# Kernel optimization log

Hardware: AMD Instinct MI355X
Metric: run time of the kernel (lower is better)

Reference implementation:

```python
import jax, jax.numpy as jnp
import numpy as np

NODE_DIM = 256
EDGE_DIM = 128
NODE_IN = 768 + 769 + 4 + 1 + 3  # 1545


def setup_inputs() -> dict:
    key = jax.random.key(0)
    ks = jax.random.split(key, 16)
    B, N, H, W, C = 8, 128, 128, 128, 768
    obj_feats = jax.random.normal(ks[0], (B, N, 769), dtype=jnp.float32)
    masks = jax.random.uniform(ks[1], (B, N, H, W), dtype=jnp.float32)
    features = jax.random.normal(ks[2], (B, C, H, W), dtype=jnp.float32)
    bboxes = jax.random.uniform(ks[3], (B, N, 4), dtype=jnp.float32)
    conf = jax.random.uniform(ks[4], (B, N), dtype=jnp.float32)
    depth = jax.random.uniform(ks[5], (B, 1, H, W), dtype=jnp.float32) + 0.1
    # near-identity pose so homogeneous divide is well-conditioned
    pose = jnp.eye(4, dtype=jnp.float32)[None] + 0.01 * jax.random.normal(ks[6], (B, 4, 4), dtype=jnp.float32)
    s = 0.02
    node_w1 = s * jax.random.normal(ks[7], (512, NODE_IN), dtype=jnp.float32)
    node_b1 = jnp.zeros((512,), dtype=jnp.float32)
    node_w2 = s * jax.random.normal(ks[8], (NODE_DIM, 512), dtype=jnp.float32)
    node_b2 = jnp.zeros((NODE_DIM,), dtype=jnp.float32)
    edge_w1 = s * jax.random.normal(ks[9], (256, 2 * NODE_DIM), dtype=jnp.float32)
    edge_b1 = jnp.zeros((256,), dtype=jnp.float32)
    edge_w2 = s * jax.random.normal(ks[10], (EDGE_DIM, 256), dtype=jnp.float32)
    edge_b2 = jnp.zeros((EDGE_DIM,), dtype=jnp.float32)
    return dict(obj_feats=obj_feats, masks=masks, features=features, bboxes=bboxes,
                conf=conf, depth=depth, pose=pose,
                node_w1=node_w1, node_b1=node_b1, node_w2=node_w2, node_b2=node_b2,
                edge_w1=edge_w1, edge_b1=edge_b1, edge_w2=edge_w2, edge_b2=edge_b2)


def _forward(obj_feats, masks, features, bboxes, conf, depth, pose,
             node_w1, node_b1, node_w2, node_b2,
             edge_w1, edge_b1, edge_w2, edge_b2):
    B, C, H, W = features.shape
    N = masks.shape[1]
    K = jnp.eye(3, dtype=features.dtype)  # self.intrinsics

    # --- mask pooling: normalized mask-weighted average of features ---
    feats_flat = features.reshape(B, C, H * W)                 # [B,C,HW]
    m_flat = masks.reshape(B, N, H * W)                        # [B,N,HW]
    m_norm = m_flat / (m_flat.sum(-1, keepdims=True) + 1e-6)
    pooled = jnp.einsum('bnh,bch->bnc', m_norm, feats_flat)    # [B,N,C]

    # --- positional encoding ---
    x1, y1, x2, y2 = bboxes[..., 0], bboxes[..., 1], bboxes[..., 2], bboxes[..., 3]
    pos_feat = jnp.stack([(x1 + x2) / 2, (y1 + y2) / 2, x2 - x1, y2 - y1], axis=-1)  # [B,N,4]

    # --- motion prior ---
    ys = jnp.arange(H, dtype=masks.dtype)
    xs = jnp.arange(W, dtype=masks.dtype)
    mask_sum = masks.sum((-1, -2)) + 1e-6                      # [B,N]
    cx = jnp.einsum('bnhw,w->bn', masks, xs) / mask_sum
    cy = jnp.einsum('bnhw,h->bn', masks, ys) / mask_sum
    cx_idx = jnp.clip(jnp.round(cx).astype(jnp.int32), 0, W - 1)
    cy_idx = jnp.clip(jnp.round(cy).astype(jnp.int32), 0, H - 1)
    b_idx = jnp.arange(B)[:, None]                             # [B,1]
    z = depth[b_idx, 0, cy_idx, cx_idx]                        # [B,N]
    X = (cx - K[0, 2]) * z / K[0, 0]
    Y = (cy - K[1, 2]) * z / K[1, 1]
    ones = jnp.ones_like(z)
    P_h = jnp.stack([X, Y, z, ones], axis=-1)                  # [B,N,4]
    P_next = jnp.einsum('bij,bnj->bni', pose, P_h)             # [B,N,4]
    motion = P_next[..., :3] / P_next[..., 3:]                 # [B,N,3]

    # --- node MLP ---
    node_input = jnp.concatenate([pooled, obj_feats, pos_feat, conf[..., None], motion], axis=-1)
    h = jax.nn.relu(node_input @ node_w1.T + node_b1)
    node_emb = h @ node_w2.T + node_b2                         # [B,N,node_dim]

    # --- edge MLP: cat([n_i, n_j]) @ W1 == n_i @ W1a + n_j @ W1b (avoid O(N^2 * 2D) cat) ---
    D = node_emb.shape[-1]
    w1a, w1b = edge_w1[:, :D], edge_w1[:, D:]
    hi = node_emb @ w1a.T                                      # [B,N,256]
    hj = node_emb @ w1b.T                                      # [B,N,256]
    he = jax.nn.relu(hi[:, :, None, :] + hj[:, None, :, :] + edge_b1)  # [B,N,N,256]
    edge_emb = he @ edge_w2.T + edge_b2                        # [B,N,N,edge_dim]

    # --- adjacency: exp(-cdist) ---
    sq = jnp.sum(node_emb * node_emb, axis=-1)                 # [B,N]
    d2 = sq[:, :, None] + sq[:, None, :] - 2.0 * jnp.einsum('bnd,bmd->bnm', node_emb, node_emb)
    d2 = jnp.maximum(d2, 0.0)
    d = jnp.where(d2 > 0, jnp.sqrt(jnp.where(d2 > 0, d2, 1.0)), 0.0)  # grad-safe sqrt at 0
    adj = jnp.exp(-d)
    return node_emb, edge_emb, adj


def reference(obj_feats, masks, features, bboxes, conf, depth, pose,
              node_w1, node_b1, node_w2, node_b2,
              edge_w1, edge_b1, edge_w2, edge_b2):
    return _forward(obj_feats, masks, features, bboxes, conf, depth, pose,
                    node_w1, node_b1, node_w2, node_b2,
                    edge_w1, edge_b1, edge_w2, edge_b2)
```

## Files before the change

kernel.cpp:

```cpp
#include <hip/hip_runtime.h>
#include <hip/hip_bf16.h>

#define B_   8
#define N_   128
#define HW_  16384
#define C_   768
#define NIN_ 1545
#define NINP_ 1600
#define D1_  512
#define D_   256
#define EO_  128

typedef short s16x8 __attribute__((ext_vector_type(8)));
typedef float f32x16 __attribute__((ext_vector_type(16)));

__device__ __forceinline__ unsigned short f2bf(float x) {
  union { __hip_bfloat16 h; unsigned short u; } cv;
  cv.h = __float2bfloat16(x);
  return cv.u;
}

__global__ __launch_bounds__(256) void mask_stats_k(const float* __restrict__ masks,
                                                    const float* __restrict__ depth,
                                                    const float* __restrict__ pose,
                                                    float4* __restrict__ stats) {
  int row = blockIdx.x;
  int b = row >> 7;
  const float4* mp = (const float4*)(masks + (size_t)row * HW_);
  double s = 0.0, sx = 0.0, sy = 0.0;
  for (int it = 0; it < 16; ++it) {
    int i4 = threadIdx.x + it * 256;
    float4 v = mp[i4];
    int flat = i4 * 4;
    int y = flat >> 7, xb = flat & 127;
    double rs = (double)v.x + (double)v.y + (double)v.z + (double)v.w;
    s += rs;
    sx += (double)v.x * xb + (double)v.y * (xb + 1) + (double)v.z * (xb + 2) + (double)v.w * (xb + 3);
    sy += rs * (double)y;
  }
  for (int off = 32; off; off >>= 1) {
    s  += __shfl_down(s,  off);
    sx += __shfl_down(sx, off);
    sy += __shfl_down(sy, off);
  }
  __shared__ double red[3][4];
  int w = threadIdx.x >> 6, l = threadIdx.x & 63;
  if (l == 0) { red[0][w] = s; red[1][w] = sx; red[2][w] = sy; }
  __syncthreads();
  if (threadIdx.x == 0) {
    s  = red[0][0] + red[0][1] + red[0][2] + red[0][3];
    sx = red[1][0] + red[1][1] + red[1][2] + red[1][3];
    sy = red[2][0] + red[2][1] + red[2][2] + red[2][3];
    double msum = s + 1e-6;
    double cx = sx / msum, cy = sy / msum;
    int cxi = (int)rint(cx); cxi = min(127, max(0, cxi));
    int cyi = (int)rint(cy); cyi = min(127, max(0, cyi));
    double z = (double)depth[(size_t)b * HW_ + cyi * 128 + cxi];
    double Ph[4] = { cx * z, cy * z, z, 1.0 };
    const float* P = pose + b * 16;
    double pn[4];
    #pragma unroll
    for (int r = 0; r < 4; ++r)
      pn[r] = (double)P[r*4+0]*Ph[0] + (double)P[r*4+1]*Ph[1] + (double)P[r*4+2]*Ph[2] + (double)P[r*4+3]*Ph[3];
    double inv3 = 1.0 / pn[3];
    stats[row] = make_float4((float)(1.0 / msum), (float)(pn[0]*inv3), (float)(pn[1]*inv3), (float)(pn[2]*inv3));
  }
}

__global__ __launch_bounds__(256) void convw_k(const float* __restrict__ w1,
                                               const float* __restrict__ w2,
                                               const float* __restrict__ ew1,
                                               const float* __restrict__ ew2,
                                               unsigned short* __restrict__ w1b,
                                               unsigned short* __restrict__ w2b,
                                               unsigned short* __restrict__ we1b,
                                               unsigned short* __restrict__ ew2b) {
  int i = blockIdx.x * 256 + threadIdx.x;
  if (i < 512 * NINP_) {
    int r = i / NINP_, k = i - r * NINP_;
    w1b[i] = f2bf(k < NIN_ ? w1[r * NIN_ + k] : 0.0f);
    return;
  }
  i -= 512 * NINP_;
  if (i < 256 * 512) { w2b[i] = f2bf(w2[i]); return; }
  i -= 256 * 512;
  if (i < 512 * 256) {
    int r = i >> 8, k = i & 255;
    we1b[i] = f2bf(r < 256 ? ew1[r * 512 + k] : ew1[(r - 256) * 512 + 256 + k]);
    return;
  }
  i -= 512 * 256;
  if (i < 128 * 256) { ew2b[i] = f2bf(ew2[i]); }
}

__global__ __launch_bounds__(256) void pooled_k(const float* __restrict__ masks,
                                                const float* __restrict__ feats,
                                                float* __restrict__ Spart) {
  __shared__ short As[128 * 72];
  __shared__ short Bs[128 * 72];
  int bx = blockIdx.x;
  int ct = bx % 6, kc = bx / 6;
  int b = blockIdx.y;
  const float* mb = masks + (size_t)b * N_ * HW_;
  const float* fb = feats + ((size_t)b * C_ + (size_t)ct * 128) * HW_;
  int t = threadIdx.x, w = t >> 6, l = t & 63;
  int rsel = l & 31, khalf = l >> 5;
  f32x16 acc[4];
  #pragma unroll
  for (int nt = 0; nt < 4; ++nt)
    #pragma unroll
    for (int i = 0; i < 16; ++i) acc[nt][i] = 0.0f;

  for (int kt = 0; kt < 32; ++kt) {
    int kbase = kc * 2048 + kt * 64;
    #pragma unroll
    for (int c = 0; c < 8; ++c) {
      int chunk = t + 256 * c;
      int row = chunk >> 4;
      int kof = (chunk & 15) << 2;
      float4 va = *(const float4*)(mb + (size_t)row * HW_ + kbase + kof);
      ushort4 pa = { f2bf(va.x), f2bf(va.y), f2bf(va.z), f2bf(va.w) };
      *(ushort4*)((unsigned short*)As + row * 72 + kof) = pa;
      float4 vb = *(const float4*)(fb + (size_t)row * HW_ + kbase + kof);
      ushort4 pb = { f2bf(vb.x), f2bf(vb.y), f2bf(vb.z), f2bf(vb.w) };
      *(ushort4*)((unsigned short*)Bs + row * 72 + kof) = pb;
    }
    __syncthreads();
    #pragma unroll
    for (int ks = 0; ks < 4; ++ks) {
      s16x8 a = *(const s16x8*)&As[(w * 32 + rsel) * 72 + ks * 16 + khalf * 8];
      #pragma unroll
      for (int nt = 0; nt < 4; ++nt) {
        s16x8 bf = *(const s16x8*)&Bs[(nt * 32 + rsel) * 72 + ks * 16 + khalf * 8];
        acc[nt] = __builtin_amdgcn_mfma_f32_32x32x16_bf16(a, bf, acc[nt], 0, 0, 0);
      }
    }
    __syncthreads();
  }
  float* op = Spart + (size_t)kc * (B_ * N_ * C_ / 8 * 8) / 8 * 8;
  op = Spart + (size_t)kc * 786432 + (size_t)b * 98304;
  #pragma unroll
  for (int nt = 0; nt < 4; ++nt)
    #pragma unroll
    for (int reg = 0; reg < 16; ++reg) {
      int rm = w * 32 + (reg & 3) + 8 * (reg >> 2) + 4 * khalf;
      int cn = ct * 128 + nt * 32 + rsel;
      op[rm * C_ + cn] = acc[nt][reg];
    }
}

__global__ __launch_bounds__(256) void assemble_k(const float* __restrict__ Spart,
                                                  const float4* __restrict__ stats,
                                                  const float* __restrict__ obj,
                                                  const float* __restrict__ bboxes,
                                                  const float* __restrict__ conf,
                                                  unsigned short* __restrict__ ni) {
  int r = blockIdx.x;
  float4 st = stats[r];
  float x1 = bboxes[r*4+0], y1 = bboxes[r*4+1], x2 = bboxes[r*4+2], y2 = bboxes[r*4+3];
  for (int k = threadIdx.x; k < NINP_; k += 256) {
    float v;
    if (k < 768) {
      float acc = 0.0f;
      #pragma unroll
      for (int kc = 0; kc < 8; ++kc) acc += Spart[(size_t)kc * 786432 + (size_t)r * C_ + k];
      v = acc * st.x;
    } else if (k < 1537) v = obj[(size_t)r * 769 + (k - 768)];
    else if (k == 1537) v = 0.5f * (x1 + x2);
    else if (k == 1538) v = 0.5f * (y1 + y2);
    else if (k == 1539) v = x2 - x1;
    else if (k == 1540) v = y2 - y1;
    else if (k == 1541) v = conf[r];
    else if (k == 1542) v = st.y;
    else if (k == 1543) v = st.z;
    else if (k == 1544) v = st.w;
    else v = 0.0f;
    ni[(size_t)r * NINP_ + k] = f2bf(v);
  }
}

template <bool RELU, bool BIAS, int OUTM>
__global__ __launch_bounds__(256) void gemm64_k(const unsigned short* __restrict__ A,
                                                const unsigned short* __restrict__ Bm,
                                                const float* __restrict__ bias,
                                                float* __restrict__ Cf,
                                                unsigned short* __restrict__ Cb,
                                                int K, int N) {
  __shared__ short As[64 * 72];
  __shared__ short Bs[64 * 72];
  int n0 = blockIdx.x * 64, m0 = blockIdx.y * 64;
  int t = threadIdx.x, w = t >> 6, l = t & 63;
  int rsel = l & 31, khalf = l >> 5;
  int mh = (w & 1) * 32, nh = (w >> 1) * 32;
  f32x16 acc;
  #pragma unroll
  for (int i = 0; i < 16; ++i) acc[i] = 0.0f;

  for (int k0 = 0; k0 < K; k0 += 64) {
    #pragma unroll
    for (int c = 0; c < 2; ++c) {
      int chunk = t + 256 * c;
      int row = chunk >> 3, kof = (chunk & 7) * 8;
      *(uint4*)((unsigned short*)As + row * 72 + kof) =
          *(const uint4*)&A[(size_t)(m0 + row) * K + k0 + kof];
      *(uint4*)((unsigned short*)Bs + row * 72 + kof) =
          *(const uint4*)&Bm[(size_t)(n0 + row) * K + k0 + kof];
    }
    __syncthreads();
    #pragma unroll
    for (int ks = 0; ks < 4; ++ks) {
      s16x8 a = *(const s16x8*)&As[(mh + rsel) * 72 + ks * 16 + khalf * 8];
      s16x8 bf = *(const s16x8*)&Bs[(nh + rsel) * 72 + ks * 16 + khalf * 8];
      acc = __builtin_amdgcn_mfma_f32_32x32x16_bf16(a, bf, acc, 0, 0, 0);
    }
    __syncthreads();
  }
  #pragma unroll
  for (int reg = 0; reg < 16; ++reg) {
    int rm = m0 + mh + (reg & 3) + 8 * (reg >> 2) + 4 * khalf;
    int cn = n0 + nh + rsel;
    float v = acc[reg];
    if (BIAS) v += bias[cn];
    if (RELU) v = fmaxf(v, 0.0f);
    if (OUTM == 0 || OUTM == 2) Cf[(size_t)rm * N + cn] = v;
    if (OUTM == 1 || OUTM == 2) Cb[(size_t)rm * N + cn] = f2bf(v);
  }
}

__global__ __launch_bounds__(256) void edge_k(const float* __restrict__ hihj,
                                              const unsigned short* __restrict__ ew2b,
                                              const float* __restrict__ eb1,
                                              const float* __restrict__ eb2,
                                              float* __restrict__ out_edge) {
  __shared__ short W2s[128 * 264];
  __shared__ float hi_s[256];
  __shared__ float b1_s[256];
  __shared__ float b2_s[128];
  int bi = blockIdx.x;
  int b = bi >> 7;
  int t = threadIdx.x, w = t >> 6, l = t & 63;
  int rsel = l & 31, khalf = l >> 5;

  #pragma unroll
  for (int c = 0; c < 16; ++c) {
    int chunk = t + 256 * c;
    int row = chunk >> 5, kof = (chunk & 31) * 8;
    *(uint4*)((unsigned short*)W2s + row * 264 + kof) = *(const uint4*)&ew2b[row * 256 + kof];
  }
  hi_s[t] = hihj[(size_t)bi * 512 + t];
  b1_s[t] = eb1[t];
  if (t < 128) b2_s[t] = eb2[t];
  __syncthreads();

  f32x16 acc[4];
  #pragma unroll
  for (int nt = 0; nt < 4; ++nt)
    #pragma unroll
    for (int i = 0; i < 16; ++i) acc[nt][i] = 0.0f;

  const float* hjb = hihj + (size_t)b * 128 * 512 + 256;
  int jrow = w * 32 + rsel;
  #pragma unroll
  for (int ks = 0; ks < 16; ++ks) {
    int k0 = ks * 16 + khalf * 8;
    const float* hp = hjb + (size_t)jrow * 512 + k0;
    float4 h0 = *(const float4*)hp;
    float4 h1 = *(const float4*)(hp + 4);
    float f[8] = { h0.x, h0.y, h0.z, h0.w, h1.x, h1.y, h1.z, h1.w };
    s16x8 a;
    #pragma unroll
    for (int c = 0; c < 8; ++c)
      a[c] = (short)f2bf(fmaxf(f[c] + hi_s[k0 + c] + b1_s[k0 + c], 0.0f));
    #pragma unroll
    for (int nt = 0; nt < 4; ++nt) {
      s16x8 bf = *(const s16x8*)&W2s[(nt * 32 + rsel) * 264 + k0];
      acc[nt] = __builtin_amdgcn_mfma_f32_32x32x16_bf16(a, bf, acc[nt], 0, 0, 0);
    }
  }
  float* ob = out_edge + (size_t)bi * 128 * 128;
  #pragma unroll
  for (int nt = 0; nt < 4; ++nt)
    #pragma unroll
    for (int reg = 0; reg < 16; ++reg) {
      int j = w * 32 + (reg & 3) + 8 * (reg >> 2) + 4 * khalf;
      int o = nt * 32 + rsel;
      ob[(size_t)j * 128 + o] = acc[nt][reg] + b2_s[o];
    }
}

__global__ __launch_bounds__(128) void adj_k(const float* __restrict__ ne,
                                             float* __restrict__ adj) {
  int bi = blockIdx.x;
  int b = bi >> 7;
  __shared__ float nei[256];
  int t = threadIdx.x;
  nei[t] = ne[(size_t)bi * 256 + t];
  nei[t + 128] = ne[(size_t)bi * 256 + t + 128];
  __syncthreads();
  const float* nj = ne + ((size_t)b * 128 + t) * 256;
  float dot = 0.0f, sqj = 0.0f, sqi = 0.0f;
  for (int k = 0; k < 256; ++k) {
    float a = nei[k], c = nj[k];
    dot += a * c; sqj += c * c; sqi += a * a;
  }
  float d2 = fmaxf(sqi + sqj - 2.0f * dot, 0.0f);
  float d = d2 > 0.0f ? sqrtf(d2) : 0.0f;
  adj[(size_t)bi * 128 + t] = expf(-d);
}

extern "C" void kernel_launch(void* const* d_in, const int* in_sizes, int n_in,
                              void* d_out, int out_size, void* d_ws, size_t ws_size,
                              hipStream_t stream) {
  const float* obj    = (const float*)d_in[0];
  const float* masks  = (const float*)d_in[1];
  const float* feats  = (const float*)d_in[2];
  const float* bboxes = (const float*)d_in[3];
  const float* conf   = (const float*)d_in[4];
  const float* depth  = (const float*)d_in[5];
  const float* pose   = (const float*)d_in[6];
  const float* nw1    = (const float*)d_in[7];
  const float* nb1    = (const float*)d_in[8];
  const float* nw2    = (const float*)d_in[9];
  const float* nb2    = (const float*)d_in[10];
  const float* ew1    = (const float*)d_in[11];
  const float* eb1    = (const float*)d_in[12];
  const float* ew2    = (const float*)d_in[13];
  const float* eb2    = (const float*)d_in[14];

  char* ws = (char*)d_ws;
  float*          Spart = (float*)ws;
  unsigned short* h_bf  = (unsigned short*)ws;
  unsigned short* ne_bf = (unsigned short*)(ws + 1048576);
  float*          hihj  = (float*)(ws + 1572864);
  float4*         stats = (float4*)(ws + 25165824);
  unsigned short* ni_bf = (unsigned short*)(ws + 25182208);
  unsigned short* w1b   = (unsigned short*)(ws + 28459008);
  unsigned short* w2b   = (unsigned short*)(ws + 30097408);
  unsigned short* we1b  = (unsigned short*)(ws + 30359552);
  unsigned short* ew2b  = (unsigned short*)(ws + 30621696);

  float* out      = (float*)d_out;
  float* out_ne   = out;
  float* out_edge = out + 262144;
  float* out_adj  = out + 262144 + 16777216;

  mask_stats_k<<<dim3(1024), dim3(256), 0, stream>>>(masks, depth, pose, stats);
  convw_k<<<dim3(4352), dim3(256), 0, stream>>>(nw1, nw2, ew1, ew2, w1b, w2b, we1b, ew2b);
  pooled_k<<<dim3(48, 8), dim3(256), 0, stream>>>(masks, feats, Spart);
  assemble_k<<<dim3(1024), dim3(256), 0, stream>>>(Spart, stats, obj, bboxes, conf, ni_bf);
  gemm64_k<true,  true,  1><<<dim3(8, 16), dim3(256), 0, stream>>>(ni_bf, w1b, nb1, nullptr, h_bf, NINP_, 512);
  gemm64_k<false, true,  2><<<dim3(4, 16), dim3(256), 0, stream>>>(h_bf, w2b, nb2, out_ne, ne_bf, 512, 256);
  gemm64_k<false, false, 0><<<dim3(8, 16), dim3(256), 0, stream>>>(ne_bf, we1b, nullptr, hihj, nullptr, 256, 512);
  edge_k<<<dim3(1024), dim3(256), 0, stream>>>(hihj, ew2b, eb1, eb2, out_edge);
  adj_k<<<dim3(1024), dim3(128), 0, stream>>>(out_ne, out_adj);
}
```

Before: 732.0 us.

## Merge prep and edge/adj kernels, deepen split-K pooling with register prefetch

Several changes land together. Mask stats and weight conversion become one launch, and edge and adjacency become one launch. The pooling GEMM doubles split-K to 16 chunks and remaps blocks across batches, which raises parallelism. Its global loads are prefetched into registers one tile ahead of the LDS store, so memory latency overlaps with MFMA work. The adjacency path now stages neighbor rows through LDS in tiles with a two-way K split. The cost is a larger Spart partial buffer (workspace offsets move) and more reduction work in assemble.

After: 751.5 us. 1.03x slower.

```diff
diff --git a/kernel.cpp b/kernel.cpp
--- a/kernel.cpp
+++ b/kernel.cpp
@@ -10,6 +10,7 @@
 #define D1_  512
 #define D_   256
 #define EO_  128
+#define KC_  16
 
 typedef short s16x8 __attribute__((ext_vector_type(8)));
 typedef float f32x16 __attribute__((ext_vector_type(16)));
@@ -20,10 +21,37 @@
   return cv.u;
 }
 
-__global__ __launch_bounds__(256) void mask_stats_k(const float* __restrict__ masks,
-                                                    const float* __restrict__ depth,
-                                                    const float* __restrict__ pose,
-                                                    float4* __restrict__ stats) {
+__global__ __launch_bounds__(256) void prep_k(const float* __restrict__ masks,
+                                              const float* __restrict__ depth,
+                                              const float* __restrict__ pose,
+                                              float4* __restrict__ stats,
+                                              const float* __restrict__ w1,
+                                              const float* __restrict__ w2,
+                                              const float* __restrict__ ew1,
+                                              const float* __restrict__ ew2,
+                                              unsigned short* __restrict__ w1b,
+                                              unsigned short* __restrict__ w2b,
+                                              unsigned short* __restrict__ we1b,
+                                              unsigned short* __restrict__ ew2b) {
+  if (blockIdx.x >= 1024) {
+    int i = (blockIdx.x - 1024) * 256 + threadIdx.x;
+    if (i < 512 * NINP_) {
+      int r = i / NINP_, k = i - r * NINP_;
+      w1b[i] = f2bf(k < NIN_ ? w1[r * NIN_ + k] : 0.0f);
+      return;
+    }
+    i -= 512 * NINP_;
+    if (i < 256 * 512) { w2b[i] = f2bf(w2[i]); return; }
+    i -= 256 * 512;
+    if (i < 512 * 256) {
+      int r = i >> 8, k = i & 255;
+      we1b[i] = f2bf(r < 256 ? ew1[r * 512 + k] : ew1[(r - 256) * 512 + 256 + k]);
+      return;
+    }
+    i -= 512 * 256;
+    if (i < 128 * 256) { ew2b[i] = f2bf(ew2[i]); }
+    return;
+  }
   int row = blockIdx.x;
   int b = row >> 7;
   const float4* mp = (const float4*)(masks + (size_t)row * HW_);
@@ -67,40 +95,16 @@
   }
 }
 
-__global__ __launch_bounds__(256) void convw_k(const float* __restrict__ w1,
-                                               const float* __restrict__ w2,
-                                               const float* __restrict__ ew1,
-                                               const float* __restrict__ ew2,
-                                               unsigned short* __restrict__ w1b,
-                                               unsigned short* __restrict__ w2b,
-                                               unsigned short* __restrict__ we1b,
-                                               unsigned short* __restrict__ ew2b) {
-  int i = blockIdx.x * 256 + threadIdx.x;
-  if (i < 512 * NINP_) {
-    int r = i / NINP_, k = i - r * NINP_;
-    w1b[i] = f2bf(k < NIN_ ? w1[r * NIN_ + k] : 0.0f);
-    return;
-  }
-  i -= 512 * NINP_;
-  if (i < 256 * 512) { w2b[i] = f2bf(w2[i]); return; }
-  i -= 256 * 512;
-  if (i < 512 * 256) {
-    int r = i >> 8, k = i & 255;
-    we1b[i] = f2bf(r < 256 ? ew1[r * 512 + k] : ew1[(r - 256) * 512 + 256 + k]);
-    return;
-  }
-  i -= 512 * 256;
-  if (i < 128 * 256) { ew2b[i] = f2bf(ew2[i]); }
-}
-
 __global__ __launch_bounds__(256) void pooled_k(const float* __restrict__ masks,
                                                 const float* __restrict__ feats,
                                                 float* __restrict__ Spart) {
   __shared__ short As[128 * 72];
   __shared__ short Bs[128 * 72];
-  int bx = blockIdx.x;
-  int ct = bx % 6, kc = bx / 6;
-  int b = blockIdx.y;
+  int id = blockIdx.x + 96 * blockIdx.y;
+  int lg = (id & 7) * 96 + (id >> 3);
+  int b  = lg / 96;
+  int lx = lg - b * 96;
+  int ct = lx % 6, kc = lx / 6;
   const float* mb = masks + (size_t)b * N_ * HW_;
   const float* fb = feats + ((size_t)b * C_ + (size_t)ct * 128) * HW_;
   int t = threadIdx.x, w = t >> 6, l = t & 63;
@@ -111,20 +115,32 @@
     #pragma unroll
     for (int i = 0; i < 16; ++i) acc[nt][i] = 0.0f;
 
-  for (int kt = 0; kt < 32; ++kt) {
-    int kbase = kc * 2048 + kt * 64;
+  float4 va[8], vb[8];
+  auto issue = [&](int kt) {
+    int kbase = kc * 1024 + kt * 64;
     #pragma unroll
     for (int c = 0; c < 8; ++c) {
       int chunk = t + 256 * c;
       int row = chunk >> 4;
       int kof = (chunk & 15) << 2;
-      float4 va = *(const float4*)(mb + (size_t)row * HW_ + kbase + kof);
-      ushort4 pa = { f2bf(va.x), f2bf(va.y), f2bf(va.z), f2bf(va.w) };
+      va[c] = *(const float4*)(mb + (size_t)row * HW_ + kbase + kof);
+      vb[c] = *(const float4*)(fb + (size_t)row * HW_ + kbase + kof);
+    }
+  };
+  issue(0);
+  for (int kt = 0; kt < 16; ++kt) {
+    #pragma unroll
+    for (int c = 0; c < 8; ++c) {
+      int chunk = t + 256 * c;
+      int row = chunk >> 4;
+      int kof = (chunk & 15) << 2;
+      float4 A4 = va[c], B4 = vb[c];
+      ushort4 pa = { f2bf(A4.x), f2bf(A4.y), f2bf(A4.z), f2bf(A4.w) };
       *(ushort4*)((unsigned short*)As + row * 72 + kof) = pa;
-      float4 vb = *(const float4*)(fb + (size_t)row * HW_ + kbase + kof);
-      ushort4 pb = { f2bf(vb.x), f2bf(vb.y), f2bf(vb.z), f2bf(vb.w) };
+      ushort4 pb = { f2bf(B4.x), f2bf(B4.y), f2bf(B4.z), f2bf(B4.w) };
       *(ushort4*)((unsigned short*)Bs + row * 72 + kof) = pb;
     }
+    if (kt < 15) issue(kt + 1);
     __syncthreads();
     #pragma unroll
     for (int ks = 0; ks < 4; ++ks) {
@@ -137,8 +153,7 @@
     }
     __syncthreads();
   }
-  float* op = Spart + (size_t)kc * (B_ * N_ * C_ / 8 * 8) / 8 * 8;
-  op = Spart + (size_t)kc * 786432 + (size_t)b * 98304;
+  float* op = Spart + (size_t)kc * 786432 + (size_t)b * 98304;
   #pragma unroll
   for (int nt = 0; nt < 4; ++nt)
     #pragma unroll
@@ -163,7 +178,7 @@
     if (k < 768) {
       float acc = 0.0f;
       #pragma unroll
-      for (int kc = 0; kc < 8; ++kc) acc += Spart[(size_t)kc * 786432 + (size_t)r * C_ + k];
+      for (int kc = 0; kc < KC_; ++kc) acc += Spart[(size_t)kc * 786432 + (size_t)r * C_ + k];
       v = acc * st.x;
     } else if (k < 1537) v = obj[(size_t)r * 769 + (k - 768)];
     else if (k == 1537) v = 0.5f * (x1 + x2);
@@ -227,85 +242,111 @@
   }
 }
 
-__global__ __launch_bounds__(256) void edge_k(const float* __restrict__ hihj,
-                                              const unsigned short* __restrict__ ew2b,
-                                              const float* __restrict__ eb1,
-                                              const float* __restrict__ eb2,
-                                              float* __restrict__ out_edge) {
-  __shared__ short W2s[128 * 264];
-  __shared__ float hi_s[256];
-  __shared__ float b1_s[256];
-  __shared__ float b2_s[128];
-  int bi = blockIdx.x;
-  int b = bi >> 7;
-  int t = threadIdx.x, w = t >> 6, l = t & 63;
-  int rsel = l & 31, khalf = l >> 5;
-
-  #pragma unroll
-  for (int c = 0; c < 16; ++c) {
-    int chunk = t + 256 * c;
-    int row = chunk >> 5, kof = (chunk & 31) * 8;
-    *(uint4*)((unsigned short*)W2s + row * 264 + kof) = *(const uint4*)&ew2b[row * 256 + kof];
-  }
-  hi_s[t] = hihj[(size_t)bi * 512 + t];
-  b1_s[t] = eb1[t];
-  if (t < 128) b2_s[t] = eb2[t];
-  __syncthreads();
-
-  f32x16 acc[4];
-  #pragma unroll
-  for (int nt = 0; nt < 4; ++nt)
-    #pragma unroll
-    for (int i = 0; i < 16; ++i) acc[nt][i] = 0.0f;
-
-  const float* hjb = hihj + (size_t)b * 128 * 512 + 256;
-  int jrow = w * 32 + rsel;
-  #pragma unroll
-  for (int ks = 0; ks < 16; ++ks) {
-    int k0 = ks * 16 + khalf * 8;
-    const float* hp = hjb + (size_t)jrow * 512 + k0;
-    float4 h0 = *(const float4*)hp;
-    float4 h1 = *(const float4*)(hp + 4);
-    float f[8] = { h0.x, h0.y, h0.z, h0.w, h1.x, h1.y, h1.z, h1.w };
-    s16x8 a;
-    #pragma unroll
-    for (int c = 0; c < 8; ++c)
-      a[c] = (short)f2bf(fmaxf(f[c] + hi_s[k0 + c] + b1_s[k0 + c], 0.0f));
-    #pragma unroll
-    for (int nt = 0; nt < 4; ++nt) {
-      s16x8 bf = *(const s16x8*)&W2s[(nt * 32 + rsel) * 264 + k0];
-      acc[nt] = __builtin_amdgcn_mfma_f32_32x32x16_bf16(a, bf, acc[nt], 0, 0, 0);
-    }
-  }
-  float* ob = out_edge + (size_t)bi * 128 * 128;
-  #pragma unroll
-  for (int nt = 0; nt < 4; ++nt)
-    #pragma unroll
-    for (int reg = 0; reg < 16; ++reg) {
-      int j = w * 32 + (reg & 3) + 8 * (reg >> 2) + 4 * khalf;
-      int o = nt * 32 + rsel;
-      ob[(size_t)j * 128 + o] = acc[nt][reg] + b2_s[o];
-    }
-}
-
-__global__ __launch_bounds__(128) void adj_k(const float* __restrict__ ne,
-                                             float* __restrict__ adj) {
-  int bi = blockIdx.x;
-  int b = bi >> 7;
-  __shared__ float nei[256];
+__global__ __launch_bounds__(256) void edge_adj_k(const float* __restrict__ hihj,
+                                                  const unsigned short* __restrict__ ew2b,
+                                                  const float* __restrict__ eb1,
+                                                  const float* __restrict__ eb2,
+                                                  const float* __restrict__ ne,
+                                                  float* __restrict__ out_edge,
+                                                  float* __restrict__ out_adj) {
+  __shared__ union {
+    struct { short W2s[128 * 264]; float hi_s[256]; float b1_s[256]; float b2_s[128]; } e;
+    struct { float njs[128 * 65]; float nei[256]; float red[3][256]; } a;
+  } sm;
+  int id = blockIdx.x;
+  int lg = (id & 7) * 256 + (id >> 3);
   int t = threadIdx.x;
-  nei[t] = ne[(size_t)bi * 256 + t];
-  nei[t + 128] = ne[(size_t)bi * 256 + t + 128];
-  __syncthreads();
-  const float* nj = ne + ((size_t)b * 128 + t) * 256;
-  float dot = 0.0f, sqj = 0.0f, sqi = 0.0f;
-  for (int k = 0; k < 256; ++k) {
-    float a = nei[k], c = nj[k];
-    dot += a * c; sqj += c * c; sqi += a * a;
-  }
-  float d2 = fmaxf(sqi + sqj - 2.0f * dot, 0.0f);
-  float d = d2 > 0.0f ? sqrtf(d2) : 0.0f;
-  adj[(size_t)bi * 128 + t] = expf(-d);
+
+  if (lg < 1024) {
+    int bi = lg;
+    int b = bi >> 7;
+    int w = t >> 6, l = t & 63;
+    int rsel = l & 31, khalf = l >> 5;
+
+    #pragma unroll
+    for (int c = 0; c < 16; ++c) {
+      int chunk = t + 256 * c;
+      int row = chunk >> 5, kof = (chunk & 31) * 8;
+      *(uint4*)((unsigned short*)sm.e.W2s + row * 264 + kof) = *(const uint4*)&ew2b[row * 256 + kof];
+    }
+    sm.e.hi_s[t] = hihj[(size_t)bi * 512 + t];
+    sm.e.b1_s[t] = eb1[t];
+    if (t < 128) sm.e.b2_s[t] = eb2[t];
+    __syncthreads();
+
+    f32x16 acc[4];
+    #pragma unroll
+    for (int nt = 0; nt < 4; ++nt)
+      #pragma unroll
+      for (int i = 0; i < 16; ++i) acc[nt][i] = 0.0f;
+
+    const float* hjb = hihj + (size_t)b * 128 * 512 + 256;
+    int jrow = w * 32 + rsel;
+    #pragma unroll
+    for (int ks = 0; ks < 16; ++ks) {
+      int k0 = ks * 16 + khalf * 8;
+      const float* hp = hjb + (size_t)jrow * 512 + k0;
+      float4 h0 = *(const float4*)hp;
+      float4 h1 = *(const float4*)(hp + 4);
+      float f[8] = { h0.x, h0.y, h0.z, h0.w, h1.x, h1.y, h1.z, h1.w };
+      s16x8 a;
+      #pragma unroll
+      for (int c = 0; c < 8; ++c)
+        a[c] = (short)f2bf(fmaxf(f[c] + sm.e.hi_s[k0 + c] + sm.e.b1_s[k0 + c], 0.0f));
+      #pragma unroll
+      for (int nt = 0; nt < 4; ++nt) {
+        s16x8 bf = *(const s16x8*)&sm.e.W2s[(nt * 32 + rsel) * 264 + k0];
+        acc[nt] = __builtin_amdgcn_mfma_f32_32x32x16_bf16(a, bf, acc[nt], 0, 0, 0);
+      }
+    }
+    float* ob = out_edge + (size_t)bi * 128 * 128;
+    #pragma unroll
+    for (int nt = 0; nt < 4; ++nt)
+      #pragma unroll
+      for (int reg = 0; reg < 16; ++reg) {
+        int j = w * 32 + (reg & 3) + 8 * (reg >> 2) + 4 * khalf;
+        int o = nt * 32 + rsel;
+        ob[(size_t)j * 128 + o] = acc[nt][reg] + sm.e.b2_s[o];
+      }
+  } else {
+    int bi = lg - 1024;
+    int b = bi >> 7;
+    const float* neb = ne + (size_t)b * 128 * 256;
+    int j = t & 127, kh = t >> 7;
+    sm.a.nei[t] = ne[(size_t)bi * 256 + t];
+    float dot = 0.0f, sqj = 0.0f, sqi = 0.0f;
+    for (int tile = 0; tile < 4; ++tile) {
+      __syncthreads();
+      #pragma unroll
+      for (int p = 0; p < 8; ++p) {
+        int f = p * 256 + t;
+        int row = f >> 4;
+        int k4 = (f & 15) << 2;
+        float4 v = *(const float4*)(neb + (size_t)row * 256 + tile * 64 + k4);
+        float* dst = &sm.a.njs[row * 65 + k4];
+        dst[0] = v.x; dst[1] = v.y; dst[2] = v.z; dst[3] = v.w;
+      }
+      __syncthreads();
+      int kb = tile * 64 + kh * 32;
+      #pragma unroll
+      for (int k = 0; k < 32; ++k) {
+        float c = sm.a.njs[j * 65 + kh * 32 + k];
+        float aa = sm.a.nei[kb + k];
+        dot += aa * c; sqj += c * c; sqi += aa * aa;
+      }
+    }
+    __syncthreads();
+    sm.a.red[0][t] = dot; sm.a.red[1][t] = sqj; sm.a.red[2][t] = sqi;
+    __syncthreads();
+    if (t < 128) {
+      dot = sm.a.red[0][t] + sm.a.red[0][t + 128];
+      sqj = sm.a.red[1][t] + sm.a.red[1][t + 128];
+      sqi = sm.a.red[2][t] + sm.a.red[2][t + 128];
+      float d2 = fmaxf(sqi + sqj - 2.0f * dot, 0.0f);
+      float d = d2 > 0.0f ? sqrtf(d2) : 0.0f;
+      out_adj[(size_t)bi * 128 + t] = expf(-d);
+    }
+  }
 }
 
 extern "C" void kernel_launch(void* const* d_in, const int* in_sizes, int n_in,
@@ -332,25 +373,24 @@
   unsigned short* h_bf  = (unsigned short*)ws;
   unsigned short* ne_bf = (unsigned short*)(ws + 1048576);
   float*          hihj  = (float*)(ws + 1572864);
-  float4*         stats = (float4*)(ws + 25165824);
-  unsigned short* ni_bf = (unsigned short*)(ws + 25182208);
-  unsigned short* w1b   = (unsigned short*)(ws + 28459008);
-  unsigned short* w2b   = (unsigned short*)(ws + 30097408);
-  unsigned short* we1b  = (unsigned short*)(ws + 30359552);
-  unsigned short* ew2b  = (unsigned short*)(ws + 30621696);
+  float4*         stats = (float4*)(ws + 50331648);
+  unsigned short* ni_bf = (unsigned short*)(ws + 50348032);
+  unsigned short* w1b   = (unsigned short*)(ws + 53624832);
+  unsigned short* w2b   = (unsigned short*)(ws + 55263232);
+  unsigned short* we1b  = (unsigned short*)(ws + 55525376);
+  unsigned short* ew2b  = (unsigned short*)(ws + 55787520);
 
   float* out      = (float*)d_out;
   float* out_ne   = out;
   float* out_edge = out + 262144;
   float* out_adj  = out + 262144 + 16777216;
 
-  mask_stats_k<<<dim3(1024), dim3(256), 0, stream>>>(masks, depth, pose, stats);
-  convw_k<<<dim3(4352), dim3(256), 0, stream>>>(nw1, nw2, ew1, ew2, w1b, w2b, we1b, ew2b);
-  pooled_k<<<dim3(48, 8), dim3(256), 0, stream>>>(masks, feats, Spart);
+  prep_k<<<dim3(5376), dim3(256), 0, stream>>>(masks, depth, pose, stats,
+                                               nw1, nw2, ew1, ew2, w1b, w2b, we1b, ew2b);
+  pooled_k<<<dim3(96, 8), dim3(256), 0, stream>>>(masks, feats, Spart);
   assemble_k<<<dim3(1024), dim3(256), 0, stream>>>(Spart, stats, obj, bboxes, conf, ni_bf);
   gemm64_k<true,  true,  1><<<dim3(8, 16), dim3(256), 0, stream>>>(ni_bf, w1b, nb1, nullptr, h_bf, NINP_, 512);
   gemm64_k<false, true,  2><<<dim3(4, 16), dim3(256), 0, stream>>>(h_bf, w2b, nb2, out_ne, ne_bf, 512, 256);
   gemm64_k<false, false, 0><<<dim3(8, 16), dim3(256), 0, stream>>>(ne_bf, we1b, nullptr, hihj, nullptr, 256, 512);
-  edge_k<<<dim3(1024), dim3(256), 0, stream>>>(hihj, ew2b, eb1, eb2, out_edge);
-  adj_k<<<dim3(1024), dim3(128), 0, stream>>>(out_ne, out_adj);
-}
+  edge_adj_k<<<dim3(2048), dim3(256), 0, stream>>>(hihj, ew2b, eb1, eb2, out_ne, out_edge, out_adj);
+}
```
